# Optimization experiments

Measured on AMD Instinct MI355X. Metric: run time of the kernel, lower is better.

Reference implementation:

```python
import jax, jax.numpy as jnp
from jax import lax
import numpy as np

H = W = 32          # feature map size (1024px image / stride 32)
A = 9               # 3 scales x 3 ratios
IOU_THR = 0.5
DN = ('NCHW', 'OIHW', 'NCHW')


def _base_anchors():
    scales = [8.0, 16.0, 32.0]
    ratios = [0.5, 1.0, 2.0]
    rows = []
    for s in scales:
        for r in ratios:
            w = s * np.sqrt(r)
            h = s / np.sqrt(r)
            rows.append([-w / 2, -h / 2, w / 2, h / 2])
    return jnp.asarray(np.array(rows, dtype=np.float32))  # [A,4]


def setup_inputs() -> dict:
    key = jax.random.key(0)
    ks = jax.random.split(key, 4)
    x = jax.random.normal(ks[0], (1, 2048, H, W), jnp.float32)
    # small weight scale keeps exp(dw) in a sane range, like a trained RPN
    conv_w = jax.random.normal(ks[1], (512, 2048, 3, 3), jnp.float32) * 0.01
    conv_b = jnp.zeros((512,), jnp.float32)
    cls_w = jax.random.normal(ks[2], (2 * A, 512, 1, 1), jnp.float32) * 0.01
    cls_b = jnp.zeros((2 * A,), jnp.float32)
    bbox_w = jax.random.normal(ks[3], (4 * A, 512, 1, 1), jnp.float32) * 0.01
    bbox_b = jnp.zeros((4 * A,), jnp.float32)
    return {"x": x, "conv_w": conv_w, "conv_b": conv_b,
            "cls_w": cls_w, "cls_b": cls_b, "bbox_w": bbox_w, "bbox_b": bbox_b}


def _conv(x, w, b, pad):
    y = lax.conv_general_dilated(x, w, (1, 1), pad, dimension_numbers=DN)
    return y + b[None, :, None, None]


def _pairwise_iou(boxes):
    # boxes: [N,4] (x1,y1,x2,y2)
    area = (boxes[:, 2] - boxes[:, 0]) * (boxes[:, 3] - boxes[:, 1])
    lt = jnp.maximum(boxes[:, None, :2], boxes[None, :, :2])
    rb = jnp.minimum(boxes[:, None, 2:], boxes[None, :, 2:])
    wh = jnp.clip(rb - lt, 0.0)
    inter = wh[..., 0] * wh[..., 1]
    union = area[:, None] + area[None, :] - inter
    return inter / jnp.maximum(union, 1e-9)


def _nms_keep(boxes_sorted):
    # boxes sorted by descending score; sequential greedy suppression
    n = boxes_sorted.shape[0]
    iou = _pairwise_iou(boxes_sorted)  # [N,N]
    idx = jnp.arange(n)
    def body(i, keep):
        sup = (iou[i] > IOU_THR) & (idx > i) & keep[i]
        return keep & ~sup
    return lax.fori_loop(0, n, body, jnp.ones((n,), bool))


def _rpn_forward(x, conv_w, conv_b, cls_w, cls_b, bbox_w, bbox_b):
    feat = jax.nn.relu(_conv(x, conv_w, conv_b, 'SAME'))            # [1,512,H,W]
    obj = _conv(feat, cls_w, cls_b, 'VALID')                        # [1,18,H,W]
    deltas = _conv(feat, bbox_w, bbox_b, 'VALID')                   # [1,36,H,W]

    # softmax over the 2 classes (torch view(B,2,-1): first 9 channels = class 0)
    probs = jax.nn.softmax(obj[0].reshape(2, -1), axis=0)[1]        # [A*H*W] anchor-major
    scores = probs.reshape(A, H, W).transpose(1, 2, 0).reshape(-1)  # (pos, anchor) order

    # bbox channel layout: channel = a*4 + coord (0::4 slicing in torch)
    d = deltas[0].reshape(A, 4, H, W).transpose(2, 3, 0, 1).reshape(-1, 4)  # [N,4]

    anchors = jnp.tile(_base_anchors(), (H * W, 1))                 # [N,4], pos*9+a
    aw = anchors[:, 2] - anchors[:, 0]
    ah = anchors[:, 3] - anchors[:, 1]
    cx = anchors[:, 0] + 0.5 * aw
    cy = anchors[:, 1] + 0.5 * ah
    px = cx + d[:, 0] * aw
    py = cy + d[:, 1] * ah
    pw = jnp.exp(d[:, 2]) * aw
    ph = jnp.exp(d[:, 3]) * ah
    boxes = jnp.stack([px - 0.5 * pw, py - 0.5 * ph,
                       px + 0.5 * pw, py + 0.5 * ph], axis=1)       # [N,4]

    order = jnp.argsort(-scores)
    boxes_s = boxes[order]
    scores_s = scores[order]
    keep = _nms_keep(boxes_s)
    final_boxes = jnp.where(keep[:, None], boxes_s, 0.0)
    final_scores = jnp.where(keep, scores_s, 0.0)
    return final_boxes, final_scores


def reference(x, conv_w, conv_b, cls_w, cls_b, bbox_w, bbox_b):
    return _rpn_forward(x, conv_w, conv_b, cls_w, cls_b, bbox_w, bbox_b)
```

## Files before the change

kernel.cpp:

```cpp
#include <hip/hip_runtime.h>
#include <cstdint>
#include <cmath>

#define HH 32
#define WW 32
#define NPX 1024
#define CIN 2048
#define CMID 512
#define NA 9
#define NBOX 9216
#define NWRD 144

typedef double f64x4 __attribute__((ext_vector_type(4)));

#if defined(__HIP_DEVICE_COMPILE__)
#if __has_builtin(__builtin_amdgcn_mfma_f64_16x16x4f64)
#define MFMA64(a, b, c) __builtin_amdgcn_mfma_f64_16x16x4f64((a), (b), (c), 0, 0, 0)
#elif __has_builtin(__builtin_amdgcn_mfma_f64_16x16x4_f64)
#define MFMA64(a, b, c) __builtin_amdgcn_mfma_f64_16x16x4_f64((a), (b), (c), 0, 0, 0)
#endif
#endif

__global__ void k_probe(int* __restrict__ flag) {
#ifdef MFMA64
  const int lane = threadIdx.x & 63;
  const int q = lane >> 4, n16 = lane & 15;
  f64x4 z = {0.0, 0.0, 0.0, 0.0};
  f64x4 d1 = MFMA64((double)(n16 + 1), (n16 == 0) ? 1.0 : 0.0, z);
  f64x4 d2 = MFMA64(1.0, (double)(n16 + 1), z);
  bool ok0 = true, ok1 = true, ok2 = true, ok3 = true;
#pragma unroll
  for (int r = 0; r < 4; ++r) {
    const double rc = (double)(4 * q + r + 1);
    const double rs = (double)(q + 4 * r + 1);
    const double p1 = d1[r], p2 = d2[r];
    const double colv = 4.0 * (double)(n16 + 1);
    ok0 &= (p1 == ((n16 == 0) ? 4.0 * rc : 0.0)) && (p2 == colv);
    ok1 &= (p1 == ((n16 == 0) ? 4.0 * rs : 0.0)) && (p2 == colv);
    ok2 &= (p1 == ((4 * q + r == 0) ? colv : 0.0)) && (p2 == 4.0 * rc);
    ok3 &= (p1 == ((q + 4 * r == 0) ? colv : 0.0)) && (p2 == 4.0 * rs);
  }
  const unsigned long long full = ~0ull;
  int f = 0;
  if (__ballot(ok0) == full) f = 1;
  else if (__ballot(ok1) == full) f = 2;
  else if (__ballot(ok2) == full) f = 3;
  else if (__ballot(ok3) == full) f = 4;
  if (threadIdx.x == 0) *flag = f;
#else
  if (threadIdx.x == 0) *flag = 0;
#endif
}

__global__ __launch_bounds__(256) void k_conv3x3_mfma(
    const float* __restrict__ x, const float* __restrict__ wgt,
    double* __restrict__ partial, int chunk, const int* __restrict__ flag) {
#ifdef MFMA64
  const int f = *flag;
  if (f == 0) return;
  const bool swp = (f >= 3);
  const bool contig = (f == 1) || (f == 3);

  __shared__ double xs[8][4][38];
  __shared__ float wsm[72 * 81];
  const int tid = threadIdx.x;
  const int pxt = blockIdx.x;
  const int oct = blockIdx.y;
  const int cz  = blockIdx.z;
  const int h0  = pxt * 2;
  const int oc0 = oct * 64;
  const int cbase = cz * chunk;

  const int wv   = tid >> 6;
  const int lane = tid & 63;
  const int q    = lane >> 4;
  const int n16  = lane & 15;

  f64x4 acc[4];
#pragma unroll
  for (int t = 0; t < 4; ++t) acc[t] = (f64x4){0.0, 0.0, 0.0, 0.0};

  const double* xb0 = &xs[q][0][n16];
  const float*  wb0 = &wsm[q * 81 + (wv << 4) + n16];

  float xreg[5];
  float wreg[18];

#define LOAD_STAGE(C0)                                                         \
  {                                                                            \
    _Pragma("unroll")                                                          \
    for (int k = 0; k < 5; ++k) {                                              \
      const int idx = tid + k * 256;                                           \
      float v = 0.f;                                                           \
      if (idx < 1152) {                                                        \
        const int cc = idx / 144, rem = idx - cc * 144;                        \
        const int r = rem / 36, lcol = rem - r * 36;                           \
        const int grow = h0 - 1 + r, gcol = lcol - 1;                          \
        if ((unsigned)grow < 32u && (unsigned)gcol < 32u)                      \
          v = x[((size_t)((C0) + cc) << 10) + (grow << 5) + gcol];             \
      }                                                                        \
      xreg[k] = v;                                                             \
    }                                                                          \
    _Pragma("unroll")                                                          \
    for (int k = 0; k < 18; ++k) {                                             \
      const int idx = tid + k * 256;                                           \
      const int oc_l = idx / 72, rem = idx - oc_l * 72;                        \
      wreg[k] = wgt[(size_t)(oc0 + oc_l) * 18432 + (size_t)(C0) * 9 + rem];    \
    }                                                                          \
  }

  const int nst = chunk >> 3;
  LOAD_STAGE(cbase)

  for (int s = 0; s < nst; ++s) {
    __syncthreads();
#pragma unroll
    for (int k = 0; k < 5; ++k) {
      const int idx = tid + k * 256;
      if (idx < 1152) {
        const int cc = idx / 144, rem = idx - cc * 144;
        const int r = rem / 36, lcol = rem - r * 36;
        xs[cc][r][lcol] = (double)xreg[k];
      }
    }
#pragma unroll
    for (int k = 0; k < 18; ++k) {
      const int idx = tid + k * 256;
      const int oc_l = idx / 72, rem = idx - oc_l * 72;
      const int cc = rem / 9, tap = rem - cc * 9;
      wsm[(tap * 8 + cc) * 81 + oc_l] = wreg[k];
    }
    __syncthreads();
    if (s + 1 < nst) LOAD_STAGE(cbase + (s + 1) * 8)

#define CONV_INNER(SWPV)                                                       \
    _Pragma("unroll")                                                          \
    for (int tap = 0; tap < 9; ++tap) {                                        \
      const int dy = tap / 3, dx = tap - 3 * (tap / 3);                        \
      _Pragma("unroll")                                                        \
      for (int ksg = 0; ksg < 2; ++ksg) {                                      \
        const double av = (double)wb0[(tap * 8 + ksg * 4) * 81];               \
        const double* xb = xb0 + ksg * 608;            \
        _Pragma("unroll")                                                      \
        for (int t = 0; t < 4; ++t) {                                          \
          const double bv = xb[((t >> 1) + dy) * 38 + (t & 1) * 16 + dx];      \
          if (SWPV) acc[t] = MFMA64(bv, av, acc[t]);                           \
          else      acc[t] = MFMA64(av, bv, acc[t]);                           \
        }                                                                      \
      }                                                                        \
    }

    if (swp) { CONV_INNER(true) } else { CONV_INNER(false) }
#undef CONV_INNER
  }
#undef LOAD_STAGE
  double* out = partial + (size_t)cz * (CMID * NPX);
#pragma unroll
  for (int t = 0; t < 4; ++t) {
    const int px = ((h0 + (t >> 1)) << 5) + ((t & 1) << 4) + n16;
#pragma unroll
    for (int j = 0; j < 4; ++j) {
      const int row = contig ? ((q << 2) + j) : (q + (j << 2));
      const int oc = oc0 + (wv << 4) + row;
      out[(size_t)oc * NPX + px] = acc[t][j];
    }
  }
#endif
}

__global__ __launch_bounds__(256) void k_conv3x3_valu(
    const float* __restrict__ x, const float* __restrict__ wgt,
    double* __restrict__ partial, int chunk, const int* __restrict__ flag) {
  if (*flag != 0) return;
  __shared__ double xs[8][4][36];
  __shared__ double ws_s[8 * 9 * 66];
  const int tid = threadIdx.x;
  const int pxt = blockIdx.x;
  const int oct = blockIdx.y;
  const int cz  = blockIdx.z;
  const int h0  = pxt * 2;
  const int oc0 = oct * 64;
  const int cbase = cz * chunk;

  const int g   = tid & 15;
  const int ty  = tid >> 4;
  const int r_p = g >> 3;
  const int gc  = (g & 7) * 4;

  double acc[4][4];
#pragma unroll
  for (int a = 0; a < 4; ++a)
#pragma unroll
    for (int b = 0; b < 4; ++b) acc[a][b] = 0.0;

  const int stages = chunk >> 3;
  for (int s = 0; s < stages; ++s) {
    const int c0 = cbase + s * 8;
    __syncthreads();
    for (int idx = tid; idx < 1152; idx += 256) {
      int cc = idx / 144, rem = idx - cc * 144;
      int r = rem / 36, lcol = rem - r * 36;
      int grow = h0 - 1 + r, gcol = lcol - 1;
      float v = 0.f;
      if ((unsigned)grow < 32u && (unsigned)gcol < 32u)
        v = x[((size_t)(c0 + cc) << 10) + (grow << 5) + gcol];
      xs[cc][r][lcol] = (double)v;
    }
    for (int idx = tid; idx < 4608; idx += 256) {
      int oc_l = idx / 72, rem = idx - oc_l * 72;
      int cc = rem / 9, t = rem - cc * 9;
      ws_s[(cc * 9 + t) * 66 + oc_l] =
          (double)wgt[(size_t)(oc0 + oc_l) * 18432 + (size_t)(c0 + cc) * 9 + t];
    }
    __syncthreads();
    for (int cc = 0; cc < 8; ++cc) {
      double xr[3][8];
#pragma unroll
      for (int dy = 0; dy < 3; ++dy) {
        const double* xp = &xs[cc][r_p + dy][gc];
#pragma unroll
        for (int k = 0; k < 8; ++k) xr[dy][k] = xp[k];
      }
#pragma unroll
      for (int t = 0; t < 9; ++t) {
        const int dy = t / 3, dx = t - dy * 3;
        const double* wp = &ws_s[(cc * 9 + t) * 66 + ty * 4];
        const double w0 = wp[0], w1 = wp[1], w2 = wp[2], w3 = wp[3];
#pragma unroll
        for (int i = 0; i < 4; ++i) {
          const double xv = xr[dy][i + dx];
          acc[0][i] += w0 * xv;
          acc[1][i] += w1 * xv;
          acc[2][i] += w2 * xv;
          acc[3][i] += w3 * xv;
        }
      }
    }
  }
  const int pxg = (h0 + r_p) * 32 + gc;
  double* out = partial + (size_t)cz * (CMID * NPX);
#pragma unroll
  for (int j = 0; j < 4; ++j)
#pragma unroll
    for (int i = 0; i < 4; ++i)
      out[(size_t)(oc0 + ty * 4 + j) * NPX + pxg + i] = acc[j][i];
}

__global__ void k_reduce(const double* __restrict__ partial,
                         const float* __restrict__ bias,
                         double* __restrict__ feat, int S) {
  int idx = blockIdx.x * 256 + threadIdx.x;
  double s = (double)bias[idx >> 10];
  for (int z = 0; z < S; ++z) s += partial[(size_t)z * (CMID * NPX) + idx];
  feat[idx] = fmax(s, 0.0);
}

__global__ void k_1x1(const double* __restrict__ feat,
                      const float* __restrict__ cls_w, const float* __restrict__ cls_b,
                      const float* __restrict__ bbox_w, const float* __restrict__ bbox_b,
                      double* __restrict__ logits) {
  int px = blockIdx.x * 256 + threadIdx.x;
  int ch = blockIdx.y;
  const float* wv;
  float bias;
  if (ch < 18) { wv = cls_w + (size_t)ch * 512; bias = cls_b[ch]; }
  else         { wv = bbox_w + (size_t)(ch - 18) * 512; bias = bbox_b[ch - 18]; }
  double acc = 0.0;
  for (int c = 0; c < 512; ++c)
    acc += feat[((size_t)c << 10) + px] * (double)wv[c];
  logits[((size_t)ch << 10) + px] = acc + (double)bias;
}

__global__ void k_score_box(const double* __restrict__ logits,
                            double* __restrict__ scores, double* __restrict__ boxes) {
  int i = blockIdx.x * 256 + threadIdx.x;
  int pos = i / 9, a = i - pos * 9;
  const double* obj = logits;
  const double* dl  = logits + 18 * NPX;
  double l0 = obj[a * NPX + pos], l1 = obj[(9 + a) * NPX + pos];
  double delta = l1 - l0;
  scores[i] = 1.0 / (1.0 + exp(-delta));
  double d0 = dl[(a * 4 + 0) * NPX + pos], d1 = dl[(a * 4 + 1) * NPX + pos];
  double d2 = dl[(a * 4 + 2) * NPX + pos], d3 = dl[(a * 4 + 3) * NPX + pos];
  const double s_arr[3] = {8.0, 16.0, 32.0};
  const double r_arr[3] = {0.5, 1.0, 2.0};
  double sA = s_arr[a / 3], rA = r_arr[a % 3];
  double aw = (double)(float)(sA * sqrt(rA));
  double ah = (double)(float)(sA / sqrt(rA));
  double px_ = d0 * aw, py_ = d1 * ah;
  double pw = exp(d2) * aw, ph = exp(d3) * ah;
  boxes[i * 4 + 0] = px_ - 0.5 * pw;
  boxes[i * 4 + 1] = py_ - 0.5 * ph;
  boxes[i * 4 + 2] = px_ + 0.5 * pw;
  boxes[i * 4 + 3] = py_ + 0.5 * ph;
}

__global__ void k_rank_count(const double* __restrict__ scores, int* __restrict__ rank) {
  __shared__ double sj[256];
  int i  = blockIdx.x * 256 + threadIdx.x;
  int jb = blockIdx.y * 256;
  sj[threadIdx.x] = scores[jb + threadIdx.x];
  __syncthreads();
  double si = scores[i];
  int cnt = 0;
  for (int t = 0; t < 256; ++t) {
    double s = sj[t];
    int j = jb + t;
    cnt += (int)((s > si) || (s == si && j < i));
  }
  if (cnt) atomicAdd(&rank[i], cnt);
}

__global__ void k_scatter(const double* __restrict__ scores, const double* __restrict__ boxes,
                          const int* __restrict__ rank,
                          double* __restrict__ scores_s, double* __restrict__ boxes_s) {
  int i = blockIdx.x * 256 + threadIdx.x;
  int r = rank[i];
  scores_s[r] = scores[i];
  boxes_s[r * 4 + 0] = boxes[i * 4 + 0];
  boxes_s[r * 4 + 1] = boxes[i * 4 + 1];
  boxes_s[r * 4 + 2] = boxes[i * 4 + 2];
  boxes_s[r * 4 + 3] = boxes[i * 4 + 3];
}

__global__ void k_mask(const double* __restrict__ boxes_s, unsigned long long* __restrict__ mask) {
  __shared__ double jb[256][4];
  __shared__ double ib[64][4];
  const int tid = threadIdx.x;
  const int j0 = blockIdx.x * 256;
  const int i0 = blockIdx.y * 64;
  for (int idx = tid; idx < 1024; idx += 256) jb[idx >> 2][idx & 3] = boxes_s[j0 * 4 + idx];
  for (int idx = tid; idx < 256; idx += 256) ib[idx >> 2][idx & 3] = boxes_s[i0 * 4 + idx];
  __syncthreads();
  const int il = tid >> 2;
  const int i  = i0 + il;
  const int wq = blockIdx.x * 4 + (tid & 3);
  const int jlb = (tid & 3) * 64;
  double ix1 = ib[il][0], iy1 = ib[il][1], ix2 = ib[il][2], iy2 = ib[il][3];
  double iarea = (ix2 - ix1) * (iy2 - iy1);
  unsigned long long m = 0ull;
  for (int b = 0; b < 64; ++b) {
    int j = wq * 64 + b;
    double jx1 = jb[jlb + b][0], jy1 = jb[jlb + b][1];
    double jx2 = jb[jlb + b][2], jy2 = jb[jlb + b][3];
    double xx1 = fmax(ix1, jx1), yy1 = fmax(iy1, jy1);
    double xx2 = fmin(ix2, jx2), yy2 = fmin(iy2, jy2);
    double iw = fmax(xx2 - xx1, 0.0), ih = fmax(yy2 - yy1, 0.0);
    double inter = iw * ih;
    double jarea = (jx2 - jx1) * (jy2 - jy1);
    double uni = fmax(iarea + jarea - inter, 1e-9);
    bool sup = inter > 0.5 * uni;
    if (sup && j > i) m |= (1ull << b);
  }
  mask[(size_t)i * NWRD + wq] = m;
}

__global__ void k_nms_scan(const unsigned long long* __restrict__ mask,
                           int* __restrict__ keep) {
  __shared__ unsigned long long remv[NWRD];
  __shared__ int curi;
  const int tid = threadIdx.x;
  for (int i = tid; i < NBOX; i += 256) keep[i] = 0;
  if (tid < NWRD) remv[tid] = 0ull;
  __syncthreads();
  for (int w = 0; w < NWRD; ++w) {
    int cursor = 0;
    while (true) {
      if (tid == 0) {
        unsigned long long bits = ~remv[w];
        bits = (cursor >= 64) ? 0ull : (bits & (~0ull << cursor));
        curi = bits ? (w * 64 + __ffsll((long long)bits) - 1) : -1;
      }
      __syncthreads();
      int i = curi;
      __syncthreads();
      if (i < 0) break;
      if (tid == 0) keep[i] = 1;
      if (tid < NWRD) remv[tid] |= mask[(size_t)i * NWRD + tid];
      cursor = (i & 63) + 1;
      __syncthreads();
    }
  }
}

__global__ void k_finalize(const double* __restrict__ boxes_s, const double* __restrict__ scores_s,
                           const int* __restrict__ keep, float* __restrict__ out) {
  int r = blockIdx.x * 256 + threadIdx.x;
  int k = keep[r];
  out[r * 4 + 0] = k ? (float)boxes_s[r * 4 + 0] : 0.f;
  out[r * 4 + 1] = k ? (float)boxes_s[r * 4 + 1] : 0.f;
  out[r * 4 + 2] = k ? (float)boxes_s[r * 4 + 2] : 0.f;
  out[r * 4 + 3] = k ? (float)boxes_s[r * 4 + 3] : 0.f;
  out[NBOX * 4 + r] = k ? (float)scores_s[r] : 0.f;
}

static inline size_t alignup(size_t v, size_t a) { return (v + a - 1) & ~(a - 1); }

extern "C" void kernel_launch(void* const* d_in, const int* in_sizes, int n_in,
                              void* d_out, int out_size, void* d_ws, size_t ws_size,
                              hipStream_t stream) {
  const float* x      = (const float*)d_in[0];
  const float* conv_w = (const float*)d_in[1];
  const float* conv_b = (const float*)d_in[2];
  const float* cls_w  = (const float*)d_in[3];
  const float* cls_b  = (const float*)d_in[4];
  const float* bbox_w = (const float*)d_in[5];
  const float* bbox_b = (const float*)d_in[6];
  float* out = (float*)d_out;

  char* ws = (char*)d_ws;
  size_t off = 0;
  int* flag = (int*)(ws + off); off = alignup(off + 256, 256);
  unsigned long long* mask = (unsigned long long*)(ws + off); off = alignup(off + (size_t)NBOX * NWRD * 8, 256);
  double* feat     = (double*)(ws + off); off = alignup(off + (size_t)CMID * NPX * 8, 256);
  double* logits   = (double*)(ws + off); off = alignup(off + (size_t)54 * NPX * 8, 256);
  double* scores   = (double*)(ws + off); off = alignup(off + (size_t)NBOX * 8, 256);
  double* boxes    = (double*)(ws + off); off = alignup(off + (size_t)NBOX * 32, 256);
  double* scores_s = (double*)(ws + off); off = alignup(off + (size_t)NBOX * 8, 256);
  double* boxes_s  = (double*)(ws + off); off = alignup(off + (size_t)NBOX * 32, 256);
  int*   rank      = (int*)(ws + off);    off = alignup(off + (size_t)NBOX * 4, 256);
  int*   keep      = (int*)(ws + off);    off = alignup(off + (size_t)NBOX * 4, 256);
  size_t fixed = off;

  int S = 8;
  while (S > 1 && fixed + (size_t)S * CMID * NPX * 8 > ws_size) S >>= 1;
  double* partial = (double*)(ws + fixed);

  const int chunk = CIN / S;

  hipLaunchKernelGGL(k_probe, dim3(1), dim3(64), 0, stream, flag);
  hipLaunchKernelGGL(k_conv3x3_mfma, dim3(16, 8, S), dim3(256), 0, stream,
                     x, conv_w, partial, chunk, flag);
  hipLaunchKernelGGL(k_conv3x3_valu, dim3(16, 8, S), dim3(256), 0, stream,
                     x, conv_w, partial, chunk, flag);
  hipLaunchKernelGGL(k_reduce, dim3((CMID * NPX) / 256), dim3(256), 0, stream,
                     partial, conv_b, feat, S);
  hipLaunchKernelGGL(k_1x1, dim3(4, 54), dim3(256), 0, stream,
                     feat, cls_w, cls_b, bbox_w, bbox_b, logits);
  hipLaunchKernelGGL(k_score_box, dim3(NBOX / 256), dim3(256), 0, stream,
                     logits, scores, boxes);
  hipMemsetAsync(rank, 0, (size_t)NBOX * 4, stream);
  hipLaunchKernelGGL(k_rank_count, dim3(36, 36), dim3(256), 0, stream, scores, rank);
  hipLaunchKernelGGL(k_scatter, dim3(NBOX / 256), dim3(256), 0, stream,
                     scores, boxes, rank, scores_s, boxes_s);
  hipLaunchKernelGGL(k_mask, dim3(36, 144), dim3(256), 0, stream, boxes_s, mask);
  hipLaunchKernelGGL(k_nms_scan, dim3(1), dim3(256), 0, stream, mask, keep);
  hipLaunchKernelGGL(k_finalize, dim3(NBOX / 256), dim3(256), 0, stream,
                     boxes_s, scores_s, keep, out);
}
```

Measured before the change: 652.5 us.

## Double-buffer conv LDS, skip lower-triangle mask blocks, single-wave register NMS scan

The MFMA conv kernel now uses two LDS buffers with padded strides, so it writes the next stage after compute and needs one barrier per stage instead of two. The mask kernel skips IoU work for words lying entirely at or below the diagonal. The NMS scan becomes a single 64-lane wave that holds the removal bitmask in registers and finds the next kept box with a shuffle min-reduction, removing per-step block barriers. Keep is zeroed with a memset instead. The price is twice the LDS per block, which may lower occupancy, and a sequential scan that does a global-memory mask load per kept box.

After: 631.5 us. 3.2% less time.

```diff
diff --git a/kernel.cpp b/kernel.cpp
--- a/kernel.cpp
+++ b/kernel.cpp
@@ -61,8 +61,8 @@
   const bool swp = (f >= 3);
   const bool contig = (f == 1) || (f == 3);
 
-  __shared__ double xs[8][4][38];
-  __shared__ float wsm[72 * 81];
+  __shared__ double xs[2][8 * 153];
+  __shared__ float  wsm[2][72 * 73];
   const int tid = threadIdx.x;
   const int pxt = blockIdx.x;
   const int oct = blockIdx.y;
@@ -79,9 +79,6 @@
   f64x4 acc[4];
 #pragma unroll
   for (int t = 0; t < 4; ++t) acc[t] = (f64x4){0.0, 0.0, 0.0, 0.0};
-
-  const double* xb0 = &xs[q][0][n16];
-  const float*  wb0 = &wsm[q * 81 + (wv << 4) + n16];
 
   float xreg[5];
   float wreg[18];
@@ -109,29 +106,38 @@
     }                                                                          \
   }
 
+#define WRITE_STAGE(P)                                                         \
+  {                                                                            \
+    _Pragma("unroll")                                                          \
+    for (int k = 0; k < 5; ++k) {                                              \
+      const int idx = tid + k * 256;                                           \
+      if (idx < 1152) {                                                        \
+        const int cc = idx / 144, rem = idx - cc * 144;                        \
+        const int r = rem / 36, lcol = rem - r * 36;                           \
+        xs[P][cc * 153 + r * 38 + lcol] = (double)xreg[k];                     \
+      }                                                                        \
+    }                                                                          \
+    _Pragma("unroll")                                                          \
+    for (int k = 0; k < 18; ++k) {                                             \
+      const int idx = tid + k * 256;                                           \
+      const int oc_l = idx / 72, rem = idx - oc_l * 72;                        \
+      const int cc = rem / 9, tap = rem - cc * 9;                              \
+      wsm[P][(tap * 8 + cc) * 73 + oc_l] = wreg[k];                            \
+    }                                                                          \
+  }
+
   const int nst = chunk >> 3;
   LOAD_STAGE(cbase)
+  WRITE_STAGE(0)
+  __syncthreads();
 
   for (int s = 0; s < nst; ++s) {
-    __syncthreads();
-#pragma unroll
-    for (int k = 0; k < 5; ++k) {
-      const int idx = tid + k * 256;
-      if (idx < 1152) {
-        const int cc = idx / 144, rem = idx - cc * 144;
-        const int r = rem / 36, lcol = rem - r * 36;
-        xs[cc][r][lcol] = (double)xreg[k];
-      }
-    }
-#pragma unroll
-    for (int k = 0; k < 18; ++k) {
-      const int idx = tid + k * 256;
-      const int oc_l = idx / 72, rem = idx - oc_l * 72;
-      const int cc = rem / 9, tap = rem - cc * 9;
-      wsm[(tap * 8 + cc) * 81 + oc_l] = wreg[k];
-    }
-    __syncthreads();
+    const int p = s & 1;
     if (s + 1 < nst) LOAD_STAGE(cbase + (s + 1) * 8)
+    __builtin_amdgcn_sched_barrier(0);
+
+    const double* xb = &xs[p][q * 153 + n16];
+    const float*  wb = &wsm[p][q * 73 + (wv << 4) + n16];
 
 #define CONV_INNER(SWPV)                                                       \
     _Pragma("unroll")                                                          \
@@ -139,11 +145,11 @@
       const int dy = tap / 3, dx = tap - 3 * (tap / 3);                        \
       _Pragma("unroll")                                                        \
       for (int ksg = 0; ksg < 2; ++ksg) {                                      \
-        const double av = (double)wb0[(tap * 8 + ksg * 4) * 81];               \
-        const double* xb = xb0 + ksg * 608;            \
+        const double av = (double)wb[(tap * 8 + ksg * 4) * 73];                \
+        const double* xq = xb + ksg * 612;                     \
         _Pragma("unroll")                                                      \
         for (int t = 0; t < 4; ++t) {                                          \
-          const double bv = xb[((t >> 1) + dy) * 38 + (t & 1) * 16 + dx];      \
+          const double bv = xq[((t >> 1) + dy) * 38 + (t & 1) * 16 + dx];      \
           if (SWPV) acc[t] = MFMA64(bv, av, acc[t]);                           \
           else      acc[t] = MFMA64(av, bv, acc[t]);                           \
         }                                                                      \
@@ -152,8 +158,14 @@
 
     if (swp) { CONV_INNER(true) } else { CONV_INNER(false) }
 #undef CONV_INNER
+
+    if (s + 1 < nst) {
+      WRITE_STAGE(p ^ 1)
+      __syncthreads();
+    }
   }
 #undef LOAD_STAGE
+#undef WRITE_STAGE
   double* out = partial + (size_t)cz * (CMID * NPX);
 #pragma unroll
   for (int t = 0; t < 4; ++t) {
@@ -336,50 +348,57 @@
   const int i  = i0 + il;
   const int wq = blockIdx.x * 4 + (tid & 3);
   const int jlb = (tid & 3) * 64;
-  double ix1 = ib[il][0], iy1 = ib[il][1], ix2 = ib[il][2], iy2 = ib[il][3];
-  double iarea = (ix2 - ix1) * (iy2 - iy1);
   unsigned long long m = 0ull;
-  for (int b = 0; b < 64; ++b) {
-    int j = wq * 64 + b;
-    double jx1 = jb[jlb + b][0], jy1 = jb[jlb + b][1];
-    double jx2 = jb[jlb + b][2], jy2 = jb[jlb + b][3];
-    double xx1 = fmax(ix1, jx1), yy1 = fmax(iy1, jy1);
-    double xx2 = fmin(ix2, jx2), yy2 = fmin(iy2, jy2);
-    double iw = fmax(xx2 - xx1, 0.0), ih = fmax(yy2 - yy1, 0.0);
-    double inter = iw * ih;
-    double jarea = (jx2 - jx1) * (jy2 - jy1);
-    double uni = fmax(iarea + jarea - inter, 1e-9);
-    bool sup = inter > 0.5 * uni;
-    if (sup && j > i) m |= (1ull << b);
+  if (wq * 64 + 63 > i) {
+    double ix1 = ib[il][0], iy1 = ib[il][1], ix2 = ib[il][2], iy2 = ib[il][3];
+    double iarea = (ix2 - ix1) * (iy2 - iy1);
+    for (int b = 0; b < 64; ++b) {
+      int j = wq * 64 + b;
+      double jx1 = jb[jlb + b][0], jy1 = jb[jlb + b][1];
+      double jx2 = jb[jlb + b][2], jy2 = jb[jlb + b][3];
+      double xx1 = fmax(ix1, jx1), yy1 = fmax(iy1, jy1);
+      double xx2 = fmin(ix2, jx2), yy2 = fmin(iy2, jy2);
+      double iw = fmax(xx2 - xx1, 0.0), ih = fmax(yy2 - yy1, 0.0);
+      double inter = iw * ih;
+      double jarea = (jx2 - jx1) * (jy2 - jy1);
+      double uni = fmax(iarea + jarea - inter, 1e-9);
+      bool sup = inter > 0.5 * uni;
+      if (sup && j > i) m |= (1ull << b);
+    }
   }
   mask[(size_t)i * NWRD + wq] = m;
 }
 
 __global__ void k_nms_scan(const unsigned long long* __restrict__ mask,
                            int* __restrict__ keep) {
-  __shared__ unsigned long long remv[NWRD];
-  __shared__ int curi;
-  const int tid = threadIdx.x;
-  for (int i = tid; i < NBOX; i += 256) keep[i] = 0;
-  if (tid < NWRD) remv[tid] = 0ull;
-  __syncthreads();
-  for (int w = 0; w < NWRD; ++w) {
-    int cursor = 0;
-    while (true) {
-      if (tid == 0) {
-        unsigned long long bits = ~remv[w];
-        bits = (cursor >= 64) ? 0ull : (bits & (~0ull << cursor));
-        curi = bits ? (w * 64 + __ffsll((long long)bits) - 1) : -1;
-      }
-      __syncthreads();
-      int i = curi;
-      __syncthreads();
-      if (i < 0) break;
-      if (tid == 0) keep[i] = 1;
-      if (tid < NWRD) remv[tid] |= mask[(size_t)i * NWRD + tid];
-      cursor = (i & 63) + 1;
-      __syncthreads();
-    }
+  const int l = threadIdx.x & 63;
+  unsigned long long r0 = 0ull, r1 = 0ull, r2 = (l < 16) ? 0ull : ~0ull;
+  const int w0 = l, w1 = l + 64, w2 = l + 128;
+  int prev = -1;
+  while (true) {
+    int cand = 1 << 30;
+    unsigned long long b;
+    b = ~r0;
+    if (w0 * 64 <= prev) b = (w0 * 64 + 63 <= prev) ? 0ull : (b & (~0ull << (prev + 1 - w0 * 64)));
+    if (b) cand = w0 * 64 + __ffsll((long long)b) - 1;
+    b = ~r1;
+    if (w1 * 64 <= prev) b = (w1 * 64 + 63 <= prev) ? 0ull : (b & (~0ull << (prev + 1 - w1 * 64)));
+    if (b) { int c = w1 * 64 + __ffsll((long long)b) - 1; cand = c < cand ? c : cand; }
+    b = ~r2;
+    if (w2 * 64 <= prev) b = (w2 * 64 + 63 <= prev) ? 0ull : (b & (~0ull << (prev + 1 - w2 * 64)));
+    if (b) { int c = w2 * 64 + __ffsll((long long)b) - 1; cand = c < cand ? c : cand; }
+#pragma unroll
+    for (int off = 32; off; off >>= 1) {
+      int o = __shfl_xor(cand, off);
+      cand = o < cand ? o : cand;
+    }
+    if (cand >= NBOX) break;
+    const int i = cand;
+    if (l == 0) keep[i] = 1;
+    r0 |= mask[(size_t)i * NWRD + w0];
+    r1 |= mask[(size_t)i * NWRD + w1];
+    if (l < 16) r2 |= mask[(size_t)i * NWRD + w2];
+    prev = i;
   }
 }
 
@@ -440,11 +459,12 @@
   hipLaunchKernelGGL(k_score_box, dim3(NBOX / 256), dim3(256), 0, stream,
                      logits, scores, boxes);
   hipMemsetAsync(rank, 0, (size_t)NBOX * 4, stream);
+  hipMemsetAsync(keep, 0, (size_t)NBOX * 4, stream);
   hipLaunchKernelGGL(k_rank_count, dim3(36, 36), dim3(256), 0, stream, scores, rank);
   hipLaunchKernelGGL(k_scatter, dim3(NBOX / 256), dim3(256), 0, stream,
                      scores, boxes, rank, scores_s, boxes_s);
   hipLaunchKernelGGL(k_mask, dim3(36, 144), dim3(256), 0, stream, boxes_s, mask);
-  hipLaunchKernelGGL(k_nms_scan, dim3(1), dim3(256), 0, stream, mask, keep);
+  hipLaunchKernelGGL(k_nms_scan, dim3(1), dim3(64), 0, stream, mask, keep);
   hipLaunchKernelGGL(k_finalize, dim3(NBOX / 256), dim3(256), 0, stream,
                      boxes_s, scores_s, keep, out);
 }
```
